# Optimization experiments

Measured on AMD Instinct MI355X. Metric: run time of the kernel, lower is better.

The kernel has to match this reference:

```python
import jax, jax.numpy as jnp
import numpy as np

NUM_HEADS = 16
NUM_KV_HEADS = 4
HEAD_DIM = 128
EPS = 1e-6


def _rotate_half(x):
    x1, x2 = jnp.split(x, 2, axis=-1)
    return jnp.concatenate((-x2, x1), axis=-1)


def _rms_norm(x, w):
    var = jnp.mean(x * x, axis=-1, keepdims=True)
    return x * jax.lax.rsqrt(var + EPS) * w


def setup_inputs() -> dict:
    key = jax.random.key(0)
    ks = jax.random.split(key, 6)
    B, S, H = 2, 2048, 2048
    hidden_states = jax.random.normal(ks[0], (B, S, H), dtype=jnp.float32)
    # real RoPE tables (HF-style: freqs tiled twice along last dim)
    inv_freq = 1.0 / (10000.0 ** (np.arange(0, HEAD_DIM, 2, dtype=np.float32) / HEAD_DIM))
    pos = np.arange(S, dtype=np.float32)
    ang = np.concatenate([pos[:, None] * inv_freq[None, :]] * 2, axis=-1)  # [S, head_dim]
    cos = jnp.broadcast_to(jnp.cos(ang)[None], (B, S, HEAD_DIM)).astype(jnp.float32)
    sin = jnp.broadcast_to(jnp.sin(ang)[None], (B, S, HEAD_DIM)).astype(jnp.float32)
    sc = 0.02
    Wq = jax.random.normal(ks[1], (NUM_HEADS * HEAD_DIM, H), dtype=jnp.float32) * sc
    Wk = jax.random.normal(ks[2], (NUM_KV_HEADS * HEAD_DIM, H), dtype=jnp.float32) * sc
    Wv = jax.random.normal(ks[3], (NUM_KV_HEADS * HEAD_DIM, H), dtype=jnp.float32) * sc
    Wo = jax.random.normal(ks[4], (H, NUM_HEADS * HEAD_DIM), dtype=jnp.float32) * sc
    q_norm_w = jnp.ones((HEAD_DIM,), dtype=jnp.float32)
    k_norm_w = jnp.ones((HEAD_DIM,), dtype=jnp.float32)
    return {"hidden_states": hidden_states, "cos": cos, "sin": sin,
            "Wq": Wq, "Wk": Wk, "Wv": Wv, "Wo": Wo,
            "q_norm_w": q_norm_w, "k_norm_w": k_norm_w}


def reference(hidden_states, cos, sin, Wq, Wk, Wv, Wo, q_norm_w, k_norm_w):
    B, S, H = hidden_states.shape
    groups = NUM_HEADS // NUM_KV_HEADS
    # projections (Linear: x @ W^T), then [B, h, S, d]
    q = (hidden_states @ Wq.T).reshape(B, S, NUM_HEADS, HEAD_DIM).transpose(0, 2, 1, 3)
    k = (hidden_states @ Wk.T).reshape(B, S, NUM_KV_HEADS, HEAD_DIM).transpose(0, 2, 1, 3)
    v = (hidden_states @ Wv.T).reshape(B, S, NUM_KV_HEADS, HEAD_DIM).transpose(0, 2, 1, 3)
    # per-head RMSNorm
    q = _rms_norm(q, q_norm_w)
    k = _rms_norm(k, k_norm_w)
    # RoPE, cos/sin broadcast over heads (unsqueeze_dim=1)
    c = cos[:, None, :, :]
    s = sin[:, None, :, :]
    q = q * c + _rotate_half(q) * s
    k = k * c + _rotate_half(k) * s
    # GQA: expand kv heads
    k = jnp.repeat(k, groups, axis=1)
    v = jnp.repeat(v, groups, axis=1)
    scale = 1.0 / jnp.sqrt(jnp.float32(HEAD_DIM))
    scores = jnp.einsum('bhqd,bhkd->bhqk', q, k) * scale
    attn = jax.nn.softmax(scores, axis=-1)
    out = jnp.einsum('bhqk,bhkd->bhqd', attn, v)
    out = out.transpose(0, 2, 1, 3).reshape(B, S, NUM_HEADS * HEAD_DIM)
    return out @ Wo.T
```

## Files before the change

### kernel.cpp

```cpp
#include <hip/hip_runtime.h>
#include <hip/hip_bf16.h>
#include <stdint.h>

typedef __attribute__((ext_vector_type(8))) short short8;
typedef __attribute__((ext_vector_type(4))) float floatx4;
typedef __attribute__((ext_vector_type(16))) float floatx16;

#define MFMA16(a, b, c) __builtin_amdgcn_mfma_f32_16x16x32_bf16(a, b, c, 0, 0, 0)
#define MFMA32(a, b, c) __builtin_amdgcn_mfma_f32_32x32x16_bf16(a, b, c, 0, 0, 0)

static __device__ __forceinline__ void gload_lds16(const __hip_bfloat16* g, __hip_bfloat16* l) {
  __builtin_amdgcn_global_load_lds(
      (const __attribute__((address_space(1))) void*)g,
      (__attribute__((address_space(3))) void*)l,
      16, 0, 0);
}

__global__ void f2bf(const float* __restrict__ in, __hip_bfloat16* __restrict__ out, int n) {
  const int stride = gridDim.x * blockDim.x * 4;
  for (int i = (blockIdx.x * blockDim.x + threadIdx.x) * 4; i < n; i += stride) {
    const float4 v = *(const float4*)(in + i);
    __hip_bfloat16 t[4] = {__float2bfloat16(v.x), __float2bfloat16(v.y),
                           __float2bfloat16(v.z), __float2bfloat16(v.w)};
    *(short4*)(out + i) = *(const short4*)t;
  }
}

template <typename OUT_T>
__global__ __launch_bounds__(256)
void gemm_bt(const __hip_bfloat16* __restrict__ A, const __hip_bfloat16* __restrict__ Bt,
             OUT_T* __restrict__ C, int M, int N, int K) {
  __shared__ __hip_bfloat16 As[2][128 * 32];
  __shared__ __hip_bfloat16 Bs[2][128 * 32];
  const int tid = threadIdx.x;
  const int wid = tid >> 6, lane = tid & 63;
  const int lg = lane >> 4, lr = lane & 15;
  const int wr = wid >> 1, wc = wid & 1;
  const int m0 = blockIdx.x * 128, n0 = blockIdx.y * 128;
  const int nk = K >> 5;

  floatx4 acc[4][4];
#pragma unroll
  for (int mi = 0; mi < 4; ++mi)
#pragma unroll
    for (int ni = 0; ni < 4; ++ni) acc[mi][ni] = (floatx4)(0.0f);

  auto stage = [&](int buf, int kt) {
    const int k0 = kt << 5;
#pragma unroll
    for (int i = 0; i < 2; ++i) {
      const int e = (i * 256 + tid) * 8;
      const int row = e >> 5, col = e & 31;
      gload_lds16(A + (size_t)(m0 + row) * K + k0 + col, &As[buf][e]);
    }
#pragma unroll
    for (int i = 0; i < 2; ++i) {
      const int e = (i * 256 + tid) * 8;
      const int row = e >> 5, col = e & 31;
      gload_lds16(Bt + (size_t)(n0 + row) * K + k0 + col, &Bs[buf][e]);
    }
  };

  stage(0, 0);
  __syncthreads();

  for (int kt = 0; kt < nk; ++kt) {
    const int cur = kt & 1;
    if (kt + 1 < nk) stage(cur ^ 1, kt + 1);
    short8 af[4], bfr[4];
#pragma unroll
    for (int mi = 0; mi < 4; ++mi)
      af[mi] = *(const short8*)&As[cur][(wr * 64 + mi * 16 + lr) * 32 + lg * 8];
#pragma unroll
    for (int ni = 0; ni < 4; ++ni)
      bfr[ni] = *(const short8*)&Bs[cur][(wc * 64 + ni * 16 + lr) * 32 + lg * 8];
#pragma unroll
    for (int mi = 0; mi < 4; ++mi)
#pragma unroll
      for (int ni = 0; ni < 4; ++ni) acc[mi][ni] = MFMA16(af[mi], bfr[ni], acc[mi][ni]);
    __syncthreads();
  }

#pragma unroll
  for (int mi = 0; mi < 4; ++mi)
#pragma unroll
    for (int ni = 0; ni < 4; ++ni) {
      const int row = m0 + wr * 64 + mi * 16 + lg * 4;
      const int col = n0 + wc * 64 + ni * 16 + lr;
#pragma unroll
      for (int r = 0; r < 4; ++r) {
        C[(size_t)(row + r) * N + col] = (OUT_T)acc[mi][ni][r];
      }
    }
}

__global__ __launch_bounds__(256)
void normrope(const __hip_bfloat16* __restrict__ qkv, const float* __restrict__ cosb,
              const float* __restrict__ sinb, const float* __restrict__ qw,
              const float* __restrict__ kw, __hip_bfloat16* __restrict__ Q,
              __hip_bfloat16* __restrict__ K, __hip_bfloat16* __restrict__ V) {
  const int m = blockIdx.x;
  const int b = m >> 11, s = m & 2047;
  const int wid = threadIdx.x >> 6, lane = threadIdx.x & 63;
  const size_t qkvrow = (size_t)m * 3072;
  const float c1 = cosb[(size_t)m * 128 + lane], s1 = sinb[(size_t)m * 128 + lane];
  const float c2 = cosb[(size_t)m * 128 + lane + 64], s2 = sinb[(size_t)m * 128 + lane + 64];
  for (int h = wid * 6; h < wid * 6 + 6; ++h) {
    const float x1 = __bfloat162float(qkv[qkvrow + h * 128 + lane]);
    const float x2 = __bfloat162float(qkv[qkvrow + h * 128 + lane + 64]);
    if (h < 20) {
      float ss = x1 * x1 + x2 * x2;
      ss += __shfl_xor(ss, 1);  ss += __shfl_xor(ss, 2);  ss += __shfl_xor(ss, 4);
      ss += __shfl_xor(ss, 8);  ss += __shfl_xor(ss, 16); ss += __shfl_xor(ss, 32);
      const float rs = rsqrtf(ss * (1.0f / 128.0f) + 1e-6f);
      const float* w = (h < 16) ? qw : kw;
      const float n1 = x1 * rs * w[lane], n2 = x2 * rs * w[lane + 64];
      const float o1 = n1 * c1 - n2 * s1;
      const float o2 = n2 * c2 + n1 * s2;
      if (h < 16) {
        const size_t base = ((size_t)(b * 16 + h) * 2048 + s) * 128;
        Q[base + lane] = __float2bfloat16(o1);
        Q[base + lane + 64] = __float2bfloat16(o2);
      } else {
        const size_t base = ((size_t)(b * 4 + h - 16) * 2048 + s) * 128;
        K[base + lane] = __float2bfloat16(o1);
        K[base + lane + 64] = __float2bfloat16(o2);
      }
    } else {
      const size_t base = ((size_t)(b * 4 + h - 20) * 2048 + s) * 128;
      V[base + lane] = qkv[qkvrow + h * 128 + lane];
      V[base + lane + 64] = qkv[qkvrow + h * 128 + lane + 64];
    }
  }
}

__global__ __launch_bounds__(256)
void vtrans(const __hip_bfloat16* __restrict__ V, __hip_bfloat16* __restrict__ Vt) {
  __shared__ short L[64 * 65];
  const int tid = threadIdx.x;
  const int s0 = blockIdx.x * 64, d0 = blockIdx.y * 64, bz = blockIdx.z;
  const __hip_bfloat16* src = V + (size_t)bz * 2048 * 128;
#pragma unroll
  for (int i = 0; i < 2; ++i) {
    const int slot = i * 256 + tid;
    const int srow = slot >> 3, c8 = (slot & 7) * 8;
    short8 v = *(const short8*)(src + (size_t)(s0 + srow) * 128 + d0 + c8);
#pragma unroll
    for (int j = 0; j < 8; ++j) L[(c8 + j) * 65 + srow] = v[j];
  }
  __syncthreads();
  __hip_bfloat16* dst = Vt + (size_t)bz * 128 * 2048;
#pragma unroll
  for (int i = 0; i < 2; ++i) {
    const int slot = i * 256 + tid;
    const int drow = slot >> 3, sc8 = (slot & 7) * 8;
    short8 o;
#pragma unroll
    for (int j = 0; j < 8; ++j) o[j] = L[drow * 65 + sc8 + j];
    *(short8*)(dst + (size_t)(d0 + drow) * 2048 + s0 + sc8) = o;
  }
}

__global__ __launch_bounds__(256, 2)
void fattn(const __hip_bfloat16* __restrict__ Qg, const __hip_bfloat16* __restrict__ Kg,
           const __hip_bfloat16* __restrict__ Vtg, __hip_bfloat16* __restrict__ Og) {
  __shared__ short SMEM[17920];
  short* Ksf = SMEM;
  short* Vtl = SMEM + 8704;

  const int tid = threadIdx.x, wid = tid >> 6, lane = tid & 63;
  const int l31 = lane & 31, hi = lane >> 5;
  const int qt = blockIdx.x, bh = blockIdx.y;
  const int b = bh >> 4, h = bh & 15, hkv = h >> 2;
  const int q0w = qt * 128 + wid * 32;

  const __hip_bfloat16* Qrow = Qg + ((size_t)((b * 16 + h) * 2048 + q0w + l31)) * 128;
  short8 qf2[8];
#pragma unroll
  for (int ks = 0; ks < 8; ++ks) qf2[ks] = *(const short8*)(Qrow + ks * 16 + hi * 8);

  const __hip_bfloat16* Kbase = Kg + (size_t)(b * 4 + hkv) * 2048 * 128;
  const __hip_bfloat16* Vtbase = Vtg + (size_t)(b * 4 + hkv) * 128 * 2048;

  int koff[4], kldsoff[4], voff[4], vldsoff[4];
#pragma unroll
  for (int i = 0; i < 4; ++i) {
    const int idx = i * 256 + tid;
    const int kkv = idx >> 4, kd = (idx & 15) * 8;
    koff[i] = kkv * 128 + kd;
    kldsoff[i] = kkv * 136 + kd;
    const int vd = idx >> 3, vc = (idx & 7) * 8;
    voff[i] = vd * 2048 + vc;
    vldsoff[i] = vd * 72 + vc;
  }

  floatx16 oacc[4];
#pragma unroll
  for (int dblk = 0; dblk < 4; ++dblk) oacc[dblk] = (floatx16)(0.0f);
  floatx16 lacc = (floatx16)(0.0f);

  short8 ones;
#pragma unroll
  for (int j = 0; j < 8; ++j) ones[j] = (short)0x3F80;

  const float SC2 = 0.12753102497113446f;
  const float OFF2 = 17.31234049066756f;

  short8 kreg[4], vreg[4];
  auto loadKV = [&](int kt) {
    const __hip_bfloat16* kp = Kbase + (size_t)kt * 64 * 128;
    const __hip_bfloat16* vp = Vtbase + (size_t)kt * 64;
#pragma unroll
    for (int i = 0; i < 4; ++i) kreg[i] = *(const short8*)(kp + koff[i]);
#pragma unroll
    for (int i = 0; i < 4; ++i) vreg[i] = *(const short8*)(vp + voff[i]);
  };

  loadKV(0);

  for (int kt = 0; kt < 32; ++kt) {
    if (kt) {
      asm volatile("s_waitcnt lgkmcnt(0)" ::: "memory");
      __builtin_amdgcn_s_barrier();
      __builtin_amdgcn_sched_barrier(0);
    }
#pragma unroll
    for (int i = 0; i < 4; ++i) *(short8*)&Ksf[kldsoff[i]] = kreg[i];
#pragma unroll
    for (int i = 0; i < 4; ++i) *(short8*)&Vtl[vldsoff[i]] = vreg[i];
    if (kt + 1 < 32) loadKV(kt + 1);
    asm volatile("s_waitcnt lgkmcnt(0)" ::: "memory");
    __builtin_amdgcn_s_barrier();
    __builtin_amdgcn_sched_barrier(0);

    floatx16 st[2];
    st[0] = (floatx16)(0.0f);
    st[1] = (floatx16)(0.0f);
    __builtin_amdgcn_s_setprio(1);
#pragma unroll
    for (int ks = 0; ks < 8; ++ks) {
      const short8 kf0 = *(const short8*)&Ksf[l31 * 136 + ks * 16 + hi * 8];
      const short8 kf1 = *(const short8*)&Ksf[(32 + l31) * 136 + ks * 16 + hi * 8];
      st[0] = MFMA32(kf0, qf2[ks], st[0]);
      st[1] = MFMA32(kf1, qf2[ks], st[1]);
    }
    __builtin_amdgcn_s_setprio(0);

    int pk[2][4][2];
#pragma unroll
    for (int kvblk = 0; kvblk < 2; ++kvblk)
#pragma unroll
      for (int a = 0; a < 4; ++a)
#pragma unroll
        for (int i = 0; i < 2; ++i) {
          const float e0 = exp2f(fmaf(st[kvblk][4 * a + 2 * i], SC2, -OFF2));
          const float e1 = exp2f(fmaf(st[kvblk][4 * a + 2 * i + 1], SC2, -OFF2));
          asm("v_cvt_pk_bf16_f32 %0, %1, %2" : "=v"(pk[kvblk][a][i]) : "v"(e0), "v"(e1));
        }

#pragma unroll
    for (int kvblk = 0; kvblk < 2; ++kvblk) {
#pragma unroll
      for (int ks2 = 0; ks2 < 2; ++ks2) {
        const int x0 = pk[kvblk][2 * ks2][0], x1 = pk[kvblk][2 * ks2][1];
        const int y0 = pk[kvblk][2 * ks2 + 1][0], y1 = pk[kvblk][2 * ks2 + 1][1];
        const int sx0 = __shfl_xor(x0, 32), sx1 = __shfl_xor(x1, 32);
        const int sy0 = __shfl_xor(y0, 32), sy1 = __shfl_xor(y1, 32);
        union { int i[4]; short8 s; } u;
        u.i[0] = hi ? sy0 : x0;
        u.i[1] = hi ? sy1 : x1;
        u.i[2] = hi ? y0 : sx0;
        u.i[3] = hi ? y1 : sx1;
        const short8 pB = u.s;
        __builtin_amdgcn_s_setprio(1);
        lacc = MFMA32(ones, pB, lacc);
#pragma unroll
        for (int dblk = 0; dblk < 4; ++dblk) {
          const short8 vf =
              *(const short8*)&Vtl[(dblk * 32 + l31) * 72 + kvblk * 32 + ks2 * 16 + hi * 8];
          oacc[dblk] = MFMA32(vf, pB, oacc[dblk]);
        }
        __builtin_amdgcn_s_setprio(0);
      }
    }
  }

  asm volatile("s_waitcnt lgkmcnt(0)" ::: "memory");
  __builtin_amdgcn_s_barrier();

  const float inv = 1.0f / lacc[0];
  short* tw = SMEM + wid * 4352;
#pragma unroll
  for (int dblk = 0; dblk < 4; ++dblk)
#pragma unroll
    for (int a = 0; a < 4; ++a) {
      __hip_bfloat16 o4[4];
#pragma unroll
      for (int r = 0; r < 4; ++r) o4[r] = __float2bfloat16(oacc[dblk][4 * a + r] * inv);
      *(short4*)&tw[l31 * 136 + dblk * 32 + a * 8 + hi * 4] = *(const short4*)o4;
    }
  __hip_bfloat16* orow =
      Og + ((size_t)(b * 2048 + q0w + (lane >> 1))) * 2048 + h * 128 + (lane & 1) * 64;
  const short* trow = &tw[(lane >> 1) * 136 + (lane & 1) * 64];
#pragma unroll
  for (int c = 0; c < 8; ++c) {
    *(short8*)(orow + c * 8) = *(const short8*)(trow + c * 8);
  }
}

extern "C" void kernel_launch(void* const* d_in, const int* in_sizes, int n_in,
                              void* d_out, int out_size, void* d_ws, size_t ws_size,
                              hipStream_t stream) {
  const float* hidden = (const float*)d_in[0];
  const float* cosb = (const float*)d_in[1];
  const float* sinb = (const float*)d_in[2];
  const float* Wq = (const float*)d_in[3];
  const float* Wk = (const float*)d_in[4];
  const float* Wv = (const float*)d_in[5];
  const float* Wo = (const float*)d_in[6];
  const float* qw = (const float*)d_in[7];
  const float* kw = (const float*)d_in[8];

  char* ws = (char*)d_ws;
  __hip_bfloat16* hidden_bf = (__hip_bfloat16*)ws; ws += (size_t)4096 * 2048 * 2;
  __hip_bfloat16* wqkv = (__hip_bfloat16*)ws;      ws += (size_t)3072 * 2048 * 2;
  __hip_bfloat16* wo_bf = (__hip_bfloat16*)ws;     ws += (size_t)2048 * 2048 * 2;
  __hip_bfloat16* qkv = (__hip_bfloat16*)ws;       ws += (size_t)4096 * 3072 * 2;
  __hip_bfloat16* Qb = (__hip_bfloat16*)ws;        ws += (size_t)2 * 16 * 2048 * 128 * 2;
  __hip_bfloat16* Kb = (__hip_bfloat16*)ws;        ws += (size_t)2 * 4 * 2048 * 128 * 2;
  __hip_bfloat16* Vb = (__hip_bfloat16*)ws;        ws += (size_t)2 * 4 * 2048 * 128 * 2;
  __hip_bfloat16* attn = (__hip_bfloat16*)ws;      ws += (size_t)4096 * 2048 * 2;
  __hip_bfloat16* Vt = wqkv;

  f2bf<<<1024, 256, 0, stream>>>(hidden, hidden_bf, 4096 * 2048);
  f2bf<<<1024, 256, 0, stream>>>(Wq, wqkv, 2048 * 2048);
  f2bf<<<512, 256, 0, stream>>>(Wk, wqkv + (size_t)2048 * 2048, 512 * 2048);
  f2bf<<<512, 256, 0, stream>>>(Wv, wqkv + (size_t)2560 * 2048, 512 * 2048);
  f2bf<<<1024, 256, 0, stream>>>(Wo, wo_bf, 2048 * 2048);

  gemm_bt<__hip_bfloat16><<<dim3(32, 24), 256, 0, stream>>>(hidden_bf, wqkv, qkv, 4096, 3072, 2048);
  normrope<<<4096, 256, 0, stream>>>(qkv, cosb, sinb, qw, kw, Qb, Kb, Vb);
  vtrans<<<dim3(32, 2, 8), 256, 0, stream>>>(Vb, Vt);
  fattn<<<dim3(16, 32), 256, 0, stream>>>(Qb, Kb, Vt, attn);
  gemm_bt<float><<<dim3(32, 16), 256, 0, stream>>>(attn, wo_bf, (float*)d_out, 4096, 2048, 2048);
}
```

Before: 250.7 us.

## Double-buffer K/V tiles in LDS and permute V columns to drop lane shuffles

Splits LDS into two K/V buffers so the next tile is stored while the current one is consumed, leaving one barrier per iteration instead of two. The V transpose kernel now writes its sequence columns in a permuted order that matches the MFMA accumulator layout. This lets the softmax probabilities feed the PV MFMA directly without cross-half __shfl_xor swaps. The cost is twice the LDS footprint, about 70KB per block, which may lower occupancy below the two blocks per CU the launch bounds request.

```diff
diff --git a/kernel.cpp b/kernel.cpp
--- a/kernel.cpp
+++ b/kernel.cpp
@@ -156,7 +156,12 @@
     const int drow = slot >> 3, sc8 = (slot & 7) * 8;
     short8 o;
 #pragma unroll
-    for (int j = 0; j < 8; ++j) o[j] = L[drow * 65 + sc8 + j];
+    for (int j = 0; j < 8; ++j) {
+      const int p = sc8 + j;
+      const int pb = p & 31;
+      const int phys = (p & ~31) | ((pb & 3) + ((pb >> 2) & 1) * 8 + ((pb >> 3) & 1) * 4 + (pb & 16));
+      o[j] = L[drow * 65 + phys];
+    }
     *(short8*)(dst + (size_t)(d0 + drow) * 2048 + s0 + sc8) = o;
   }
 }
@@ -164,9 +169,7 @@
 __global__ __launch_bounds__(256, 2)
 void fattn(const __hip_bfloat16* __restrict__ Qg, const __hip_bfloat16* __restrict__ Kg,
            const __hip_bfloat16* __restrict__ Vtg, __hip_bfloat16* __restrict__ Og) {
-  __shared__ short SMEM[17920];
-  short* Ksf = SMEM;
-  short* Vtl = SMEM + 8704;
+  __shared__ short SMEM[2][17920];
 
   const int tid = threadIdx.x, wid = tid >> 6, lane = tid & 63;
   const int l31 = lane & 31, hi = lane >> 5;
@@ -191,7 +194,7 @@
     kldsoff[i] = kkv * 136 + kd;
     const int vd = idx >> 3, vc = (idx & 7) * 8;
     voff[i] = vd * 2048 + vc;
-    vldsoff[i] = vd * 72 + vc;
+    vldsoff[i] = 8704 + vd * 72 + vc;
   }
 
   floatx16 oacc[4];
@@ -217,21 +220,27 @@
   };
 
   loadKV(0);
+#pragma unroll
+  for (int i = 0; i < 4; ++i) *(short8*)&SMEM[0][kldsoff[i]] = kreg[i];
+#pragma unroll
+  for (int i = 0; i < 4; ++i) *(short8*)&SMEM[0][vldsoff[i]] = vreg[i];
+  loadKV(1);
+  asm volatile("s_waitcnt lgkmcnt(0)" ::: "memory");
+  __builtin_amdgcn_s_barrier();
+  __builtin_amdgcn_sched_barrier(0);
 
   for (int kt = 0; kt < 32; ++kt) {
-    if (kt) {
-      asm volatile("s_waitcnt lgkmcnt(0)" ::: "memory");
-      __builtin_amdgcn_s_barrier();
-      __builtin_amdgcn_sched_barrier(0);
-    }
-#pragma unroll
-    for (int i = 0; i < 4; ++i) *(short8*)&Ksf[kldsoff[i]] = kreg[i];
-#pragma unroll
-    for (int i = 0; i < 4; ++i) *(short8*)&Vtl[vldsoff[i]] = vreg[i];
-    if (kt + 1 < 32) loadKV(kt + 1);
-    asm volatile("s_waitcnt lgkmcnt(0)" ::: "memory");
-    __builtin_amdgcn_s_barrier();
-    __builtin_amdgcn_sched_barrier(0);
+    const int cur = kt & 1;
+    const short* Ksf = SMEM[cur];
+    const short* Vtl = SMEM[cur];
+    if (kt + 1 < 32) {
+      short* nb = SMEM[cur ^ 1];
+#pragma unroll
+      for (int i = 0; i < 4; ++i) *(short8*)&nb[kldsoff[i]] = kreg[i];
+#pragma unroll
+      for (int i = 0; i < 4; ++i) *(short8*)&nb[vldsoff[i]] = vreg[i];
+      if (kt + 2 < 32) loadKV(kt + 2);
+    }
 
     floatx16 st[2];
     st[0] = (floatx16)(0.0f);
@@ -246,50 +255,45 @@
     }
     __builtin_amdgcn_s_setprio(0);
 
-    int pk[2][4][2];
+    int pk[2][8];
 #pragma unroll
     for (int kvblk = 0; kvblk < 2; ++kvblk)
 #pragma unroll
-      for (int a = 0; a < 4; ++a)
-#pragma unroll
-        for (int i = 0; i < 2; ++i) {
-          const float e0 = exp2f(fmaf(st[kvblk][4 * a + 2 * i], SC2, -OFF2));
-          const float e1 = exp2f(fmaf(st[kvblk][4 * a + 2 * i + 1], SC2, -OFF2));
-          asm("v_cvt_pk_bf16_f32 %0, %1, %2" : "=v"(pk[kvblk][a][i]) : "v"(e0), "v"(e1));
-        }
+      for (int m = 0; m < 8; ++m) {
+        const float e0 = exp2f(fmaf(st[kvblk][2 * m], SC2, -OFF2));
+        const float e1 = exp2f(fmaf(st[kvblk][2 * m + 1], SC2, -OFF2));
+        asm("v_cvt_pk_bf16_f32 %0, %1, %2" : "=v"(pk[kvblk][m]) : "v"(e0), "v"(e1));
+      }
 
 #pragma unroll
     for (int kvblk = 0; kvblk < 2; ++kvblk) {
 #pragma unroll
-      for (int ks2 = 0; ks2 < 2; ++ks2) {
-        const int x0 = pk[kvblk][2 * ks2][0], x1 = pk[kvblk][2 * ks2][1];
-        const int y0 = pk[kvblk][2 * ks2 + 1][0], y1 = pk[kvblk][2 * ks2 + 1][1];
-        const int sx0 = __shfl_xor(x0, 32), sx1 = __shfl_xor(x1, 32);
-        const int sy0 = __shfl_xor(y0, 32), sy1 = __shfl_xor(y1, 32);
-        union { int i[4]; short8 s; } u;
-        u.i[0] = hi ? sy0 : x0;
-        u.i[1] = hi ? sy1 : x1;
-        u.i[2] = hi ? y0 : sx0;
-        u.i[3] = hi ? y1 : sx1;
-        const short8 pB = u.s;
+      for (int s = 0; s < 2; ++s) {
+        union { int i[4]; short8 s8; } u;
+        u.i[0] = pk[kvblk][4 * s + 0];
+        u.i[1] = pk[kvblk][4 * s + 1];
+        u.i[2] = pk[kvblk][4 * s + 2];
+        u.i[3] = pk[kvblk][4 * s + 3];
+        const short8 pB = u.s8;
         __builtin_amdgcn_s_setprio(1);
         lacc = MFMA32(ones, pB, lacc);
 #pragma unroll
         for (int dblk = 0; dblk < 4; ++dblk) {
           const short8 vf =
-              *(const short8*)&Vtl[(dblk * 32 + l31) * 72 + kvblk * 32 + ks2 * 16 + hi * 8];
+              *(const short8*)&Vtl[8704 + (dblk * 32 + l31) * 72 + kvblk * 32 + s * 16 + hi * 8];
           oacc[dblk] = MFMA32(vf, pB, oacc[dblk]);
         }
         __builtin_amdgcn_s_setprio(0);
       }
     }
-  }
-
-  asm volatile("s_waitcnt lgkmcnt(0)" ::: "memory");
-  __builtin_amdgcn_s_barrier();
+
+    asm volatile("s_waitcnt lgkmcnt(0)" ::: "memory");
+    __builtin_amdgcn_s_barrier();
+    __builtin_amdgcn_sched_barrier(0);
+  }
 
   const float inv = 1.0f / lacc[0];
-  short* tw = SMEM + wid * 4352;
+  short* tw = &SMEM[0][0] + wid * 4352;
 #pragma unroll
   for (int dblk = 0; dblk < 4; ++dblk)
 #pragma unroll
```

Measured after the change: 243.5 us. 2.9% less time.
